# Optimization experiments

Measured on AMD Instinct MI355X. Metric: run time of the kernel, lower is better.

The kernel has to match this reference:

```python
import jax, jax.numpy as jnp
import numpy as np

N, T, V, D = 32, 417, 25, 2
NODES = T * V            # 10425 nodes per sample graph
E = 80000                # static interframe edges, shared across batch
HID = 20                 # GCN hidden size
LH = 50                  # lstm hidden == d_model == fc_hidden
NH, FF, NL = 5, 2048, 3  # transformer heads / ffn dim / layers
CO = 85                  # conv1d out channels (in_channels == T)
NC = 6
NS = 2                   # n stacked (lstm, gcn) stages
SZ = int(T * 0.2)        # 83 sampled timesteps for loss1
EPS = 1e-5


def setup_inputs() -> dict:
    key = jax.random.key(0)
    ks = iter(jax.random.split(key, 80))
    def r(shape, s=0.1):
        return jax.random.normal(next(ks), shape, dtype=jnp.float32) * s
    inp = {
        "x": jax.random.normal(next(ks), (N, T, V * D), dtype=jnp.float32),
        "y": jax.random.randint(next(ks), (N,), 0, NC),
        "edge_index": jax.random.randint(next(ks), (2, E), 0, NODES),
        "idx2": jax.random.randint(next(ks), (N, SZ), 0, T - 1),
        "h0s": jax.random.normal(next(ks), (NS, N, LH), dtype=jnp.float32),
        "c0s": jax.random.normal(next(ks), (NS, N, LH), dtype=jnp.float32),
        # params; layouts are (in, out) so x @ W == torch x @ W.T
        "lstm_Wih": r((NS, LH, 4 * LH)),
        "lstm_Whh": r((NS, LH, 4 * LH)),
        "lstm_bih": r((NS, 4 * LH)),
        "lstm_bhh": r((NS, 4 * LH)),
        "gcn1_W": r((NS, D, HID)),
        "gcn1_b": r((NS, HID)),
        "bn_g": jnp.ones((NS, HID), jnp.float32),
        "bn_b": jnp.zeros((NS, HID), jnp.float32),
        "gcn2_W": r((NS, HID, D)),
        "gcn2_b": r((NS, D)),
        "fc_W": r((LH, LH)),
        "fc_b": r((LH,)),
        "conv_W": r((CO, T)),
        "conv_b": r((CO,)),
        "attn_inW": r((NL, LH, 3 * LH)),
        "attn_inb": r((NL, 3 * LH)),
        "attn_outW": r((NL, LH, LH)),
        "attn_outb": r((NL, LH)),
        "ff1W": r((NL, LH, FF)),
        "ff1b": r((NL, FF)),
        "ff2W": r((NL, FF, LH)),
        "ff2b": r((NL, LH)),
        "ln1g": jnp.ones((NL, LH), jnp.float32),
        "ln1b": jnp.zeros((NL, LH), jnp.float32),
        "ln2g": jnp.ones((NL, LH), jnp.float32),
        "ln2b": jnp.zeros((NL, LH), jnp.float32),
        "Wc1": r((CO * LH, LH), 0.02),
        "bc1": r((LH,)),
        "Wc2": r((LH, NC)),
        "bc2": r((NC,)),
    }
    return inp


def _lstm(x, Wih, Whh, bih, bhh, h0, c0):
    # x: (N,T,in); single layer, batch_first; gate order i,f,g,o (torch)
    def step(carry, xt):
        h, c = carry
        g = xt @ Wih + h @ Whh + bih + bhh
        i, f, gg, o = jnp.split(g, 4, axis=-1)
        c = jax.nn.sigmoid(f) * c + jax.nn.sigmoid(i) * jnp.tanh(gg)
        h = jax.nn.sigmoid(o) * jnp.tanh(c)
        return (h, c), h
    _, hs = jax.lax.scan(step, (h0, c0), jnp.swapaxes(x, 0, 1))
    return jnp.swapaxes(hs, 0, 1)


def _gcn(X, W, b, src, dst, norm):
    # PyG GCNConv: x @ W, symmetric-normalized mean over neighbors (+self loops), + bias
    H = X @ W                                   # (N, NODES, out)
    msg = H[:, src, :] * norm[None, :, None]    # (N, E+NODES, out)
    agg = jax.vmap(lambda m: jax.ops.segment_sum(m, dst, num_segments=NODES))(msg)
    return agg + b


def _ln(x, g, b):
    m = x.mean(-1, keepdims=True)
    v = ((x - m) ** 2).mean(-1, keepdims=True)
    return (x - m) * jax.lax.rsqrt(v + EPS) * g + b


def _mha(x, inW, inb, outW, outb):
    # torch batch_first=False semantics: x is (S, B, E); here S=N, B=CO
    S, B, Em = x.shape
    hd = Em // NH
    qkv = x @ inW + inb
    q, k, v = jnp.split(qkv, 3, axis=-1)
    q = q.reshape(S, B, NH, hd)
    k = k.reshape(S, B, NH, hd)
    v = v.reshape(S, B, NH, hd)
    att = jnp.einsum('sbhd,tbhd->bhst', q, k) * (jnp.float32(hd) ** -0.5)
    w = jax.nn.softmax(att, axis=-1)
    o = jnp.einsum('bhst,tbhd->sbhd', w, v).reshape(S, B, Em)
    return o @ outW + outb


def _forward(x, y, edge_index, idx2, h0s, c0s,
             lstm_Wih, lstm_Whh, lstm_bih, lstm_bhh,
             gcn1_W, gcn1_b, bn_g, bn_b, gcn2_W, gcn2_b,
             fc_W, fc_b, conv_W, conv_b,
             attn_inW, attn_inb, attn_outW, attn_outb,
             ff1W, ff1b, ff2W, ff2b, ln1g, ln1b, ln2g, ln2b,
             Wc1, bc1, Wc2, bc2):
    loops = jnp.arange(NODES)
    src = jnp.concatenate([edge_index[0], loops])
    dst = jnp.concatenate([edge_index[1], loops])
    deg = jax.ops.segment_sum(jnp.ones(src.shape[0], jnp.float32), dst, num_segments=NODES)
    dinv = jnp.where(deg > 0, deg ** -0.5, 0.0)
    norm = dinv[src] * dinv[dst]

    x1 = x
    for s in range(NS):
        x1 = _lstm(x1, lstm_Wih[s], lstm_Whh[s], lstm_bih[s], lstm_bhh[s], h0s[s], c0s[s])
        xg = x1.reshape(N, NODES, D)
        h = _gcn(xg, gcn1_W[s], gcn1_b[s], src, dst, norm)
        # BatchNorm1d over all nodes of the whole batched graph (training stats)
        hf = h.reshape(-1, HID)
        m = hf.mean(0)
        v = hf.var(0)
        h = (h - m) * jax.lax.rsqrt(v + EPS) * bn_g[s] + bn_b[s]
        h = jax.nn.relu(h)
        xg = _gcn(h, gcn2_W[s], gcn2_b[s], src, dst, norm)
        x1 = xg.reshape(N, T, V * D)

    # unsupervised next-frame loss (Dropout is eval-mode identity)
    x_b1 = x1 @ fc_W + fc_b
    rows = jnp.arange(N)[:, None]
    pred = x_b1[rows, idx2]
    tgt = x[rows, idx2 + 1]
    loss1 = jnp.mean((pred - tgt) ** 2)

    # Conv1d(417->85, k=1) over time-as-channels
    t = jnp.einsum('oc,ncl->nol', conv_W, x1) + conv_b[None, :, None]  # (N, CO, LH)
    # torch encoder treats dim0=N as sequence, dim1=CO as batch (post-norm layers)
    for l in range(NL):
        a = _mha(t, attn_inW[l], attn_inb[l], attn_outW[l], attn_outb[l])
        t = _ln(t + a, ln1g[l], ln1b[l])
        f = jax.nn.relu(t @ ff1W[l] + ff1b[l]) @ ff2W[l] + ff2b[l]
        t = _ln(t + f, ln2g[l], ln2b[l])

    flat = t.reshape(N, CO * LH)
    h1 = jax.nn.relu(flat @ Wc1 + bc1)
    logits = h1 @ Wc2 + bc2
    logp = jax.nn.log_softmax(logits, axis=-1)
    loss2 = -jnp.mean(logp[jnp.arange(N), y])
    return jnp.exp(logp), loss1, loss2


def reference(x, y, edge_index, idx2, h0s, c0s,
              lstm_Wih, lstm_Whh, lstm_bih, lstm_bhh,
              gcn1_W, gcn1_b, bn_g, bn_b, gcn2_W, gcn2_b,
              fc_W, fc_b, conv_W, conv_b,
              attn_inW, attn_inb, attn_outW, attn_outb,
              ff1W, ff1b, ff2W, ff2b, ln1g, ln1b, ln2g, ln2b,
              Wc1, bc1, Wc2, bc2):
    return _forward(x, y, edge_index, idx2, h0s, c0s,
                    lstm_Wih, lstm_Whh, lstm_bih, lstm_bhh,
                    gcn1_W, gcn1_b, bn_g, bn_b, gcn2_W, gcn2_b,
                    fc_W, fc_b, conv_W, conv_b,
                    attn_inW, attn_inb, attn_outW, attn_outb,
                    ff1W, ff1b, ff2W, ff2b, ln1g, ln1b, ln2g, ln2b,
                    Wc1, bc1, Wc2, bc2)
```

## Files before the change

kernel.cpp:

```cpp
#include <hip/hip_runtime.h>
#include <math.h>

#define N_ 32
#define T_ 417
#define V_ 25
#define D_ 2
#define NODES_ 10425
#define E_ 80000
#define EN_ (E_ + NODES_)
#define HID_ 20
#define LH_ 50
#define NH_ 5
#define HD_ 10
#define FF_ 2048
#define NL_ 3
#define CO_ 85
#define NC_ 6
#define NS_ 2
#define SZ_ 83
#define EPS_ 1e-5f
#define NCH_ 11
#define NBNB_ 1304

__device__ inline float sane(float v){
  return (v == v && fabsf(v) < 1e30f) ? v : 0.f;
}

__device__ inline float wave_sum(float v){
  #pragma unroll
  for (int off = 32; off > 0; off >>= 1) v += __shfl_xor(v, off, 64);
  return v;
}

__global__ void k_init(const float* __restrict__ x, float* __restrict__ x1,
                       int* __restrict__ deg, float* __restrict__ accs){
  int i = blockIdx.x * 256 + threadIdx.x;
  if (i < N_*T_*LH_) x1[i] = x[i];
  if (i < NODES_) deg[i] = 0;
  if (i < 8) accs[i] = 0.f;
}

__global__ void k_deg(const int* __restrict__ ei, int* __restrict__ deg){
  int e = blockIdx.x * 256 + threadIdx.x;
  if (e >= EN_) return;
  int d = (e < E_) ? ei[E_ + e] : (e - E_);
  if ((unsigned)d >= NODES_) d = 0;
  atomicAdd(&deg[d], 1);
}

__global__ __launch_bounds__(256) void k_chunksum(const int* __restrict__ deg, int* __restrict__ csum){
  __shared__ int red[256];
  int chunk = blockIdx.x, tid = threadIdx.x;
  int s = 0;
  for (int i = tid; i < 1024; i += 256){
    int g = chunk*1024 + i;
    s += (g < NODES_) ? deg[g] : 0;
  }
  red[tid] = s;
  __syncthreads();
  for (int off = 128; off > 0; off >>= 1){
    if (tid < off) red[tid] += red[tid + off];
    __syncthreads();
  }
  if (tid == 0) csum[chunk] = red[0];
}

__global__ void k_chunkscan(int* __restrict__ csum){
  if (threadIdx.x == 0 && blockIdx.x == 0){
    int run = 0;
    for (int i = 0; i < NCH_; i++){ int t = csum[i]; csum[i] = run; run += t; }
  }
}

__global__ __launch_bounds__(1024) void k_scan2(const int* __restrict__ deg, const int* __restrict__ csum,
                       int* __restrict__ rowoff, int* __restrict__ wp, float* __restrict__ dinv){
  __shared__ int sdata[1024];
  int chunk = blockIdx.x, tid = threadIdx.x;
  int g = chunk*1024 + tid;
  int v = (g < NODES_) ? deg[g] : 0;
  int xv = v;
  sdata[tid] = xv;
  __syncthreads();
  for (int off = 1; off < 1024; off <<= 1){
    int add = (tid >= off) ? sdata[tid - off] : 0;
    __syncthreads();
    xv += add;
    sdata[tid] = xv;
    __syncthreads();
  }
  if (g < NODES_){
    int excl = csum[chunk] + xv - v;
    rowoff[g] = excl;
    wp[g] = excl;
    dinv[g] = (v > 0) ? rsqrtf((float)v) : 0.f;
  }
}

__global__ void k_scatter(const int* __restrict__ ei, const float* __restrict__ dinv,
                          int* __restrict__ wp, int* __restrict__ col, float* __restrict__ val){
  int e = blockIdx.x * 256 + threadIdx.x;
  if (e >= EN_) return;
  int s, d;
  if (e < E_){ s = ei[e]; d = ei[E_ + e]; } else { s = d = e - E_; }
  if ((unsigned)s >= NODES_) s = 0;
  if ((unsigned)d >= NODES_) d = 0;
  int pos = atomicAdd(&wp[d], 1);
  if ((unsigned)pos < EN_){
    col[pos] = s;
    val[pos] = dinv[s] * dinv[d];
  }
}

__global__ void k_xw(const float* __restrict__ x1, const float* __restrict__ Wih,
                     const float* __restrict__ bih, const float* __restrict__ bhh,
                     float* __restrict__ xW, int s){
  int idx = blockIdx.x * 256 + threadIdx.x;
  if (idx >= N_*T_*200) return;
  int r = idx / 200, g = idx % 200;
  const float* W = Wih + s*LH_*200;
  const float* xr = x1 + r*LH_;
  float acc = bih[s*200+g] + bhh[s*200+g];
  #pragma unroll 10
  for (int k = 0; k < LH_; k++) acc += xr[k] * W[k*200 + g];
  xW[idx] = acc;
}

__global__ __launch_bounds__(256) void k_lstm(const float* __restrict__ xW, float* __restrict__ x1,
                       const float* __restrict__ Whh, const float* __restrict__ h0,
                       const float* __restrict__ c0, int s){
  __shared__ float gbuf[2][200];
  int n = blockIdx.x, tid = threadIdx.x;
  int w = tid >> 6;
  int l = tid & 63;
  int li = (l < LH_) ? l : 0;
  float wcol[LH_];
  {
    const float* W = Whh + s*LH_*200 + w*LH_ + li;
    #pragma unroll
    for (int k = 0; k < LH_; k++) wcol[k] = W[k*200];
  }
  float h = 0.f, c = 0.f;
  if (l < LH_){
    h = h0[s*N_*LH_ + n*LH_ + l];
    c = c0[s*N_*LH_ + n*LH_ + l];
  }
  const float* xwn = xW + (size_t)n*T_*200;
  float* out = x1 + (size_t)n*T_*LH_;
  float xnext = (l < LH_) ? xwn[w*LH_ + li] : 0.f;
  for (int t = 0; t < T_; t++){
    float acc = xnext;
    if (t + 1 < T_) xnext = (l < LH_) ? xwn[(t+1)*200 + w*LH_ + li] : 0.f;
    #pragma unroll
    for (int k = 0; k < LH_; k++){
      float hk = __shfl(h, k, 64);
      acc += hk * wcol[k];
    }
    if (l < LH_) gbuf[t & 1][w*LH_ + l] = acc;
    __syncthreads();
    if (l < LH_){
      const float* gb = gbuf[t & 1];
      float gi = gb[l], gf = gb[LH_+l], gg = gb[100+l], go = gb[150+l];
      float si = 1.f/(1.f + __expf(-gi));
      float sf = 1.f/(1.f + __expf(-gf));
      float so = 1.f/(1.f + __expf(-go));
      float tg = tanhf(gg);
      c = sf*c + si*tg;
      h = so * tanhf(c);
      if (w == 0) out[t*LH_ + l] = h;
    }
  }
}

__global__ void k_tonode(const float* __restrict__ x1, float* __restrict__ P0){
  int idx = blockIdx.x * 256 + threadIdx.x;
  if (idx >= NODES_*64) return;
  int v = idx >> 6, rem = idx & 63;
  int n = rem >> 1, d = rem & 1;
  P0[idx] = x1[n*(T_*LH_) + v*D_ + d];
}

__global__ __launch_bounds__(64) void k_gather(const int* __restrict__ rowoff, const int* __restrict__ deg,
                       const int* __restrict__ col, const float* __restrict__ val,
                       const float* __restrict__ src, float* __restrict__ dst){
  int v = blockIdx.x, tid = threadIdx.x;
  int start = rowoff[v], len = deg[v];
  float acc = 0.f;
  for (int j = 0; j < len; j++){
    int cs = col[start + j];
    if ((unsigned)cs >= NODES_) cs = 0;
    acc += val[start + j] * src[cs*64 + tid];
  }
  dst[v*64 + tid] = acc;
}

__global__ __launch_bounds__(256) void k_bnstat(const float* __restrict__ P1, float* __restrict__ bnpart){
  int idx = blockIdx.x * 256 + threadIdx.x;
  float p0 = 0.f, p1v = 0.f;
  if (idx < NODES_*N_){ p0 = P1[idx*2]; p1v = P1[idx*2+1]; }
  float sv[5] = {p0, p1v, p0*p0, p1v*p1v, p0*p1v};
  __shared__ float red[5][4];
  int wave = threadIdx.x >> 6, lane = threadIdx.x & 63;
  #pragma unroll
  for (int j = 0; j < 5; j++){
    float w = wave_sum(sv[j]);
    if (lane == 0) red[j][wave] = w;
  }
  __syncthreads();
  if (threadIdx.x < 5){
    int j = threadIdx.x;
    bnpart[j*NBNB_ + blockIdx.x] = red[j][0] + red[j][1] + red[j][2] + red[j][3];
  }
}

__global__ __launch_bounds__(256) void k_bnfin(const float* __restrict__ bnpart,
                        const float* __restrict__ W1, const float* __restrict__ b1,
                        const float* __restrict__ bn_g, const float* __restrict__ bn_b,
                        float* __restrict__ bnsc, int s){
  __shared__ float red[256];
  __shared__ float S[5];
  int tid = threadIdx.x;
  for (int j = 0; j < 5; j++){
    float acc = 0.f;
    for (int t = tid; t < NBNB_; t += 256) acc += bnpart[j*NBNB_ + t];
    red[tid] = acc;
    __syncthreads();
    for (int off = 128; off > 0; off >>= 1){
      if (tid < off) red[tid] += red[tid + off];
      __syncthreads();
    }
    if (tid == 0) S[j] = red[0];
    __syncthreads();
  }
  if (tid < HID_){
    int c = tid;
    const float M = (float)(N_*NODES_);
    float w0 = W1[s*D_*HID_ + c], w1 = W1[s*D_*HID_ + HID_ + c];
    float bc = b1[s*HID_ + c];
    float m0 = S[0]/M, m1 = S[1]/M;
    float e00 = S[2]/M, e11 = S[3]/M, e01 = S[4]/M;
    float mean = w0*m0 + w1*m1 + bc;
    float v00 = e00 - m0*m0, v11 = e11 - m1*m1, c01 = e01 - m0*m1;
    float var = w0*w0*v00 + w1*w1*v11 + 2.f*w0*w1*c01;
    var = fmaxf(var, 0.f);
    float sc = bn_g[s*HID_ + c] * rsqrtf(var + EPS_);
    bnsc[c] = sc;
    bnsc[HID_ + c] = bn_b[s*HID_ + c] - mean*sc;
  }
}

__global__ __launch_bounds__(256) void k_bnrelu_t2(const float* __restrict__ P1, const float* __restrict__ bnsc,
                            const float* __restrict__ W1, const float* __restrict__ b1,
                            const float* __restrict__ W2, float* __restrict__ Rb, int s){
  int idx = blockIdx.x * 256 + threadIdx.x;
  if (idx >= NODES_*N_) return;
  float p0 = P1[idx*2], p1v = P1[idx*2+1];
  const float* W1p = W1 + s*D_*HID_;
  const float* W2p = W2 + s*HID_*D_;
  float a0 = 0.f, a1 = 0.f;
  #pragma unroll
  for (int c = 0; c < HID_; c++){
    float q = p0*W1p[c] + p1v*W1p[HID_ + c] + b1[s*HID_ + c];
    float h = fmaxf(q*bnsc[c] + bnsc[HID_ + c], 0.f);
    a0 += h * W2p[c*D_];
    a1 += h * W2p[c*D_ + 1];
  }
  Rb[idx*2]     = a0;
  Rb[idx*2 + 1] = a1;
}

__global__ __launch_bounds__(64) void k_gcn2(const int* __restrict__ rowoff, const int* __restrict__ deg,
                      const int* __restrict__ col, const float* __restrict__ val,
                      const float* __restrict__ Rb, const float* __restrict__ gb2,
                      float* __restrict__ x1, int s){
  int v = blockIdx.x, tid = threadIdx.x;
  int start = rowoff[v], len = deg[v];
  float acc = 0.f;
  for (int j = 0; j < len; j++){
    int cs = col[start + j];
    if ((unsigned)cs >= NODES_) cs = 0;
    acc += val[start + j] * Rb[cs*64 + tid];
  }
  int n = tid >> 1, d = tid & 1;
  x1[n*(T_*LH_) + v*D_ + d] = acc + gb2[s*D_ + d];
}

__global__ __launch_bounds__(64) void k_loss1(const float* __restrict__ x1, const float* __restrict__ x,
                       const int* __restrict__ idx2, const float* __restrict__ fcW,
                       const float* __restrict__ fcb, float* __restrict__ accs){
  int bi = blockIdx.x;
  int n = bi / SZ_, j = bi % SZ_;
  int row = idx2[n*SZ_ + j];
  if ((unsigned)row >= (T_ - 1)) row = 0;
  int l = threadIdx.x;
  float sq = 0.f;
  if (l < LH_){
    const float* xr = x1 + n*T_*LH_ + row*LH_;
    float acc = fcb[l];
    #pragma unroll 10
    for (int k = 0; k < LH_; k++) acc += xr[k] * fcW[k*LH_ + l];
    float dd = acc - x[n*T_*LH_ + (row+1)*LH_ + l];
    sq = dd*dd;
  }
  sq = wave_sum(sq);
  if (l == 0) atomicAdd(&accs[0], sq);
}

__global__ __launch_bounds__(64) void k_conv(const float* __restrict__ x1, const float* __restrict__ cW,
                      const float* __restrict__ cb, float* __restrict__ tb){
  int bi = blockIdx.x;
  int n = bi / CO_, o = bi % CO_;
  int l = threadIdx.x;
  if (l >= LH_) return;
  float acc = cb[o];
  const float* w = cW + o*T_;
  const float* xr = x1 + n*T_*LH_ + l;
  #pragma unroll 4
  for (int c2 = 0; c2 < T_; c2++) acc += w[c2] * xr[c2*LH_];
  tb[bi*LH_ + l] = acc;
}

__global__ void k_qkv(const float* __restrict__ tb, const float* __restrict__ inW,
                      const float* __restrict__ inb, float* __restrict__ qkv, int l3){
  int idx = blockIdx.x * 256 + threadIdx.x;
  if (idx >= N_*CO_*150) return;
  int r = idx / 150, j = idx % 150;
  const float* W = inW + l3*LH_*150;
  const float* tr = tb + r*LH_;
  float acc = inb[l3*150 + j];
  #pragma unroll 10
  for (int k = 0; k < LH_; k++) acc += tr[k] * W[k*150 + j];
  qkv[idx] = acc;
}

__global__ __launch_bounds__(128) void k_attn(const float* __restrict__ qkv, float* __restrict__ abuf){
  __shared__ float qs[32][HD_], ks[32][HD_], vs[32][HD_], att[32][32];
  int bi = blockIdx.x;
  int b = bi % CO_, h = bi / CO_;
  int tid = threadIdx.x;
  for (int idx = tid; idx < 960; idx += 128){
    int grp = idx / 320, m = idx % 320, ss = m / HD_, dd = m % HD_;
    float vvv = qkv[(ss*CO_ + b)*150 + grp*LH_ + h*HD_ + dd];
    if (grp == 0) qs[ss][dd] = vvv;
    else if (grp == 1) ks[ss][dd] = vvv;
    else vs[ss][dd] = vvv;
  }
  __syncthreads();
  const float scale = 0.31622776601683794f;
  for (int idx = tid; idx < 1024; idx += 128){
    int ss = idx >> 5, tt = idx & 31;
    float a = 0.f;
    #pragma unroll
    for (int dd = 0; dd < HD_; dd++) a += qs[ss][dd]*ks[tt][dd];
    att[ss][tt] = a*scale;
  }
  __syncthreads();
  if (tid < 32){
    float m = -1e31f;
    for (int tt = 0; tt < 32; tt++) m = fmaxf(m, att[tid][tt]);
    float sum = 0.f;
    for (int tt = 0; tt < 32; tt++){ float e = __expf(att[tid][tt] - m); att[tid][tt] = e; sum += e; }
    float inv = 1.f / fmaxf(sum, 1e-30f);
    for (int tt = 0; tt < 32; tt++) att[tid][tt] *= inv;
  }
  __syncthreads();
  for (int idx = tid; idx < 320; idx += 128){
    int ss = idx / HD_, dd = idx % HD_;
    float acc = 0.f;
    #pragma unroll
    for (int tt = 0; tt < 32; tt++) acc += att[ss][tt]*vs[tt][dd];
    abuf[(ss*CO_ + b)*LH_ + h*HD_ + dd] = acc;
  }
}

__global__ __launch_bounds__(64) void k_proj_ln(float* __restrict__ tb, const float* __restrict__ abuf,
                         const float* __restrict__ outW, const float* __restrict__ outb,
                         const float* __restrict__ g, const float* __restrict__ bb, int l3){
  __shared__ float orow[LH_];
  int r = blockIdx.x, l = threadIdx.x;
  if (l < LH_) orow[l] = abuf[r*LH_ + l];
  __syncthreads();
  float rr = 0.f;
  if (l < LH_){
    const float* W = outW + l3*LH_*LH_;
    float p = outb[l3*LH_ + l];
    #pragma unroll 10
    for (int k = 0; k < LH_; k++) p += orow[k] * W[k*LH_ + l];
    rr = tb[r*LH_ + l] + p;
  }
  float mean = wave_sum(rr) / (float)LH_;
  float dv = (l < LH_) ? (rr - mean) : 0.f;
  float var = wave_sum(dv*dv) / (float)LH_;
  if (l < LH_)
    tb[r*LH_ + l] = (rr - mean)*rsqrtf(var + EPS_)*g[l3*LH_ + l] + bb[l3*LH_ + l];
}

__global__ __launch_bounds__(512) void k_ff(float* __restrict__ tb, const float* __restrict__ w1,
                     const float* __restrict__ bi1, const float* __restrict__ w2,
                     const float* __restrict__ bi2, const float* __restrict__ g,
                     const float* __restrict__ bb, int l3){
  __shared__ float tin[2][LH_];
  __shared__ float hb0[FF_], hb1[FF_];
  __shared__ float part[2][8][LH_];
  int r0 = blockIdx.x * 2, tid = threadIdx.x;
  if (tid < 2*LH_) tin[tid/LH_][tid%LH_] = tb[r0*LH_ + tid];
  __syncthreads();
  const float* W1l = w1 + l3*LH_*FF_;
  #pragma unroll
  for (int i = 0; i < 4; i++){
    int j = i*512 + tid;
    float bj = bi1[l3*FF_ + j];
    float a0 = bj, a1 = bj;
    #pragma unroll 10
    for (int k = 0; k < LH_; k++){
      float w = W1l[k*FF_ + j];
      a0 += tin[0][k]*w;
      a1 += tin[1][k]*w;
    }
    hb0[j] = fmaxf(a0, 0.f);
    hb1[j] = fmaxf(a1, 0.f);
  }
  __syncthreads();
  const float* W2l = w2 + l3*FF_*LH_;
  int l = tid & 63, grp = tid >> 6;
  if (l < LH_){
    float a0 = 0.f, a1 = 0.f;
    int jbase = grp * 256;
    const float* wp = W2l + (size_t)jbase*LH_ + l;
    #pragma unroll 4
    for (int jj = 0; jj < 256; jj++){
      float w = wp[jj*LH_];
      a0 += hb0[jbase + jj]*w;
      a1 += hb1[jbase + jj]*w;
    }
    part[0][grp][l] = a0;
    part[1][grp][l] = a1;
  }
  __syncthreads();
  if (tid < 128){
    int row = tid >> 6, ll = tid & 63;
    float out = 0.f;
    if (ll < LH_){
      float a = 0.f;
      #pragma unroll
      for (int gg = 0; gg < 8; gg++) a += part[row][gg][ll];
      out = a + bi2[l3*LH_ + ll] + tin[row][ll];
    }
    float s1 = (ll < LH_) ? out : 0.f;
    float mean = wave_sum(s1) / (float)LH_;
    float dv = (ll < LH_) ? (out - mean) : 0.f;
    float var = wave_sum(dv*dv) / (float)LH_;
    if (ll < LH_)
      tb[(r0 + row)*LH_ + ll] = (out - mean)*rsqrtf(var + EPS_)*g[l3*LH_ + ll] + bb[l3*LH_ + ll];
  }
}

__global__ __launch_bounds__(512) void k_head(const float* __restrict__ tb, const int* __restrict__ y,
                       const float* __restrict__ Wc1, const float* __restrict__ bc1,
                       const float* __restrict__ Wc2, const float* __restrict__ bc2,
                       float* __restrict__ out, float* __restrict__ accs){
  __shared__ float part[8][LH_];
  __shared__ float h1[LH_];
  __shared__ float lgs[NC_];
  int n = blockIdx.x, tid = threadIdx.x;
  int l = tid & 63, grp = tid >> 6;
  const float* tr = tb + n*CO_*LH_;
  if (l < LH_){
    int k0 = grp * 532;
    int k1 = k0 + 532; if (k1 > CO_*LH_) k1 = CO_*LH_;
    float acc = 0.f;
    for (int k = k0; k < k1; k++) acc += tr[k] * Wc1[k*LH_ + l];
    part[grp][l] = acc;
  }
  __syncthreads();
  if (tid < LH_){
    float a = bc1[tid];
    #pragma unroll
    for (int gg = 0; gg < 8; gg++) a += part[gg][tid];
    h1[tid] = fmaxf(a, 0.f);
  }
  __syncthreads();
  if (tid < NC_){
    float a = bc2[tid];
    #pragma unroll 10
    for (int k = 0; k < LH_; k++) a += h1[k] * Wc2[k*NC_ + tid];
    lgs[tid] = a;
  }
  __syncthreads();
  if (tid == 0){
    float m = -1e31f;
    for (int c2 = 0; c2 < NC_; c2++) m = fmaxf(m, lgs[c2]);
    float sum = 0.f;
    for (int c2 = 0; c2 < NC_; c2++) sum += __expf(lgs[c2] - m);
    float lse = m + logf(fmaxf(sum, 1e-30f));
    for (int c2 = 0; c2 < NC_; c2++)
      out[n*NC_ + c2] = __expf(lgs[c2] - lse);
    int yy = y[n];
    if ((unsigned)yy >= NC_) yy = 0;
    atomicAdd(&accs[1], -(lgs[yy] - lse));
  }
}

__global__ void k_fin(const float* __restrict__ accs, float* __restrict__ out){
  if (threadIdx.x == 0 && blockIdx.x == 0){
    out[N_*NC_]     = sane(accs[0] / (float)(N_*SZ_*LH_));
    out[N_*NC_ + 1] = sane(accs[1] / (float)N_);
  }
}

extern "C" void kernel_launch(void* const* d_in, const int* in_sizes, int n_in,
                              void* d_out, int out_size, void* d_ws, size_t ws_size,
                              hipStream_t stream){
  static const int expect[36] = {
    667200, 32, 160000, 2656, 3200, 3200,
    20000, 20000, 400, 400,
    80, 40, 40, 40, 80, 4,
    2500, 50, 35445, 85,
    22500, 450, 7500, 150,
    307200, 6144, 307200, 150,
    150, 150, 150, 150,
    212500, 50, 300, 6
  };
  if (n_in != 36 || out_size != 194 || ws_size < 14300000) return;
  for (int i = 0; i < 36; i++) if (in_sizes[i] != expect[i]) return;

  const float* x        = (const float*)d_in[0];
  const int*   y        = (const int*)d_in[1];
  const int*   ei       = (const int*)d_in[2];
  const int*   idx2     = (const int*)d_in[3];
  const float* h0s      = (const float*)d_in[4];
  const float* c0s      = (const float*)d_in[5];
  const float* lstm_Wih = (const float*)d_in[6];
  const float* lstm_Whh = (const float*)d_in[7];
  const float* lstm_bih = (const float*)d_in[8];
  const float* lstm_bhh = (const float*)d_in[9];
  const float* gcn1_W   = (const float*)d_in[10];
  const float* gcn1_b   = (const float*)d_in[11];
  const float* bn_g     = (const float*)d_in[12];
  const float* bn_b     = (const float*)d_in[13];
  const float* gcn2_W   = (const float*)d_in[14];
  const float* gcn2_b   = (const float*)d_in[15];
  const float* fc_W     = (const float*)d_in[16];
  const float* fc_b     = (const float*)d_in[17];
  const float* conv_W   = (const float*)d_in[18];
  const float* conv_b   = (const float*)d_in[19];
  const float* attn_inW = (const float*)d_in[20];
  const float* attn_inb = (const float*)d_in[21];
  const float* attn_outW= (const float*)d_in[22];
  const float* attn_outb= (const float*)d_in[23];
  const float* ff1W     = (const float*)d_in[24];
  const float* ff1b     = (const float*)d_in[25];
  const float* ff2W     = (const float*)d_in[26];
  const float* ff2b     = (const float*)d_in[27];
  const float* ln1g     = (const float*)d_in[28];
  const float* ln1b     = (const float*)d_in[29];
  const float* ln2g     = (const float*)d_in[30];
  const float* ln2b     = (const float*)d_in[31];
  const float* Wc1      = (const float*)d_in[32];
  const float* bc1      = (const float*)d_in[33];
  const float* Wc2      = (const float*)d_in[34];
  const float* bc2      = (const float*)d_in[35];
  float* out = (float*)d_out;

  char* wsp = (char*)d_ws;
  size_t off = 0;
  auto alloc = [&](size_t bytes)->void*{
    void* p = wsp + off;
    off = (off + bytes + 255) & ~(size_t)255;
    return p;
  };
  float* x1   = (float*)alloc((size_t)N_*T_*LH_*4);
  float* X    = (float*)alloc((size_t)N_*T_*200*4);
  float* val  = (float*)alloc((size_t)EN_*4);
  float* dinv = (float*)alloc((size_t)NODES_*4);
  float* bnsc = (float*)alloc(64*4);
  float* accs = (float*)alloc(8*4);
  int*   deg  = (int*)alloc((size_t)NODES_*4);
  int*   rowoff = (int*)alloc((size_t)(NODES_+1)*4);
  int*   wp   = (int*)alloc((size_t)NODES_*4);
  int*   col  = (int*)alloc((size_t)EN_*4);
  int*   csum = (int*)alloc(16*4);
  float* xW     = X;
  float* P0     = X;
  float* P1     = X + (size_t)NODES_*64;
  float* bnpart = X + (size_t)2*NODES_*64;
  float* Rb     = P0;
  float* tb     = X;
  float* qkvb   = X + 136064;
  float* abuf   = X + 544128;

  k_init<<<dim3((N_*T_*LH_ + 255)/256), dim3(256), 0, stream>>>(x, x1, deg, accs);
  k_deg<<<dim3((EN_ + 255)/256), dim3(256), 0, stream>>>(ei, deg);
  k_chunksum<<<dim3(NCH_), dim3(256), 0, stream>>>(deg, csum);
  k_chunkscan<<<dim3(1), dim3(64), 0, stream>>>(csum);
  k_scan2<<<dim3(NCH_), dim3(1024), 0, stream>>>(deg, csum, rowoff, wp, dinv);
  k_scatter<<<dim3((EN_ + 255)/256), dim3(256), 0, stream>>>(ei, dinv, wp, col, val);

  for (int s = 0; s < NS_; s++){
    k_xw<<<dim3((N_*T_*200 + 255)/256), dim3(256), 0, stream>>>(x1, lstm_Wih, lstm_bih, lstm_bhh, xW, s);
    k_lstm<<<dim3(N_), dim3(256), 0, stream>>>(xW, x1, lstm_Whh, h0s, c0s, s);
    k_tonode<<<dim3((NODES_*64 + 255)/256), dim3(256), 0, stream>>>(x1, P0);
    k_gather<<<dim3(NODES_), dim3(64), 0, stream>>>(rowoff, deg, col, val, P0, P1);
    k_bnstat<<<dim3(NBNB_), dim3(256), 0, stream>>>(P1, bnpart);
    k_bnfin<<<dim3(1), dim3(256), 0, stream>>>(bnpart, gcn1_W, gcn1_b, bn_g, bn_b, bnsc, s);
    k_bnrelu_t2<<<dim3((N_*NODES_ + 255)/256), dim3(256), 0, stream>>>(P1, bnsc, gcn1_W, gcn1_b, gcn2_W, Rb, s);
    k_gcn2<<<dim3(NODES_), dim3(64), 0, stream>>>(rowoff, deg, col, val, Rb, gcn2_b, x1, s);
  }

  k_loss1<<<dim3(N_*SZ_), dim3(64), 0, stream>>>(x1, x, idx2, fc_W, fc_b, accs);
  k_conv<<<dim3(N_*CO_), dim3(64), 0, stream>>>(x1, conv_W, conv_b, tb);

  for (int l3 = 0; l3 < NL_; l3++){
    k_qkv<<<dim3((N_*CO_*150 + 255)/256), dim3(256), 0, stream>>>(tb, attn_inW, attn_inb, qkvb, l3);
    k_attn<<<dim3(NH_*CO_), dim3(128), 0, stream>>>(qkvb, abuf);
    k_proj_ln<<<dim3(N_*CO_), dim3(64), 0, stream>>>(tb, abuf, attn_outW, attn_outb, ln1g, ln1b, l3);
    k_ff<<<dim3(N_*CO_/2), dim3(512), 0, stream>>>(tb, ff1W, ff1b, ff2W, ff2b, ln2g, ln2b, l3);
  }

  k_head<<<dim3(N_), dim3(512), 0, stream>>>(tb, y, Wc1, bc1, Wc2, bc2, out, accs);
  k_fin<<<dim3(1), dim3(64), 0, stream>>>(accs, out);
}
```

Measured before the change: 1.676 ms.

## Replace LSTM shuffle broadcast with LDS hidden-state reads and batched output writes

```diff
diff --git a/kernel.cpp b/kernel.cpp
--- a/kernel.cpp
+++ b/kernel.cpp
@@ -128,45 +128,68 @@
 __global__ __launch_bounds__(256) void k_lstm(const float* __restrict__ xW, float* __restrict__ x1,
                        const float* __restrict__ Whh, const float* __restrict__ h0,
                        const float* __restrict__ c0, int s){
-  __shared__ float gbuf[2][200];
+  __shared__ float hsw[4][52];
+  __shared__ float gates[2][200];
+  __shared__ float hist[64][LH_];
   int n = blockIdx.x, tid = threadIdx.x;
   int w = tid >> 6;
   int l = tid & 63;
-  int li = (l < LH_) ? l : 0;
+  int gcol = (tid < 200) ? tid : 199;
   float wcol[LH_];
   {
-    const float* W = Whh + s*LH_*200 + w*LH_ + li;
+    const float* W = Whh + s*LH_*200 + gcol;
     #pragma unroll
     for (int k = 0; k < LH_; k++) wcol[k] = W[k*200];
   }
-  float h = 0.f, c = 0.f;
+  float c = 0.f;
   if (l < LH_){
-    h = h0[s*N_*LH_ + n*LH_ + l];
     c = c0[s*N_*LH_ + n*LH_ + l];
-  }
+    hsw[w][l] = h0[s*N_*LH_ + n*LH_ + l];
+  }
+  if (l >= LH_ && l < 52) hsw[w][l] = 0.f;
+  __syncthreads();
   const float* xwn = xW + (size_t)n*T_*200;
   float* out = x1 + (size_t)n*T_*LH_;
-  float xnext = (l < LH_) ? xwn[w*LH_ + li] : 0.f;
+  float xnext = (tid < 200) ? xwn[tid] : 0.f;
   for (int t = 0; t < T_; t++){
+    float hreg[52];
+    {
+      const float4* hp = (const float4*)&hsw[w][0];
+      #pragma unroll
+      for (int k4 = 0; k4 < 13; k4++){
+        float4 hv = hp[k4];
+        hreg[k4*4]   = hv.x;
+        hreg[k4*4+1] = hv.y;
+        hreg[k4*4+2] = hv.z;
+        hreg[k4*4+3] = hv.w;
+      }
+    }
     float acc = xnext;
-    if (t + 1 < T_) xnext = (l < LH_) ? xwn[(t+1)*200 + w*LH_ + li] : 0.f;
+    if (t + 1 < T_) xnext = (tid < 200) ? xwn[(t+1)*200 + tid] : 0.f;
     #pragma unroll
-    for (int k = 0; k < LH_; k++){
-      float hk = __shfl(h, k, 64);
-      acc += hk * wcol[k];
-    }
-    if (l < LH_) gbuf[t & 1][w*LH_ + l] = acc;
+    for (int k = 0; k < LH_; k++) acc += hreg[k] * wcol[k];
+    if (tid < 200) gates[t & 1][tid] = acc;
     __syncthreads();
     if (l < LH_){
-      const float* gb = gbuf[t & 1];
+      const float* gb = gates[t & 1];
       float gi = gb[l], gf = gb[LH_+l], gg = gb[100+l], go = gb[150+l];
       float si = 1.f/(1.f + __expf(-gi));
       float sf = 1.f/(1.f + __expf(-gf));
       float so = 1.f/(1.f + __expf(-go));
       float tg = tanhf(gg);
       c = sf*c + si*tg;
-      h = so * tanhf(c);
-      if (w == 0) out[t*LH_ + l] = h;
+      float h = so * tanhf(c);
+      hsw[w][l] = h;
+      if (w == 0) hist[t & 63][l] = h;
+    }
+    if ((t & 63) == 63 || t == T_ - 1){
+      __syncthreads();
+      int cnt = ((t & 63) + 1) * LH_;
+      int tbase = t - (t & 63);
+      const float* hf = &hist[0][0];
+      for (int idx = tid; idx < cnt; idx += 256)
+        out[tbase*LH_ + idx] = hf[idx];
+      __syncthreads();
     }
   }
 }
```

New measurement: 1.388 ms. -17.2%, faster.
